# Optimization experiments

Hardware: AMD Instinct MI355X
Metric: run time of the kernel (lower is better)

Reference implementation:

```python
import jax, jax.numpy as jnp
import numpy as np

N_STREAM = 5
N_ITER = 5
P_DIMS = [240, 240, 240, 240, 240]
P = sum(P_DIMS)          # 1200
B = 128
KAPPA = 0.8
LEAKY_SLOPE = 0.01       # torch nn.LeakyReLU default


def _build_masks():
    # retrive_it_mask=True: mask[i] = ones over first sum(P_DIMS[:n_stream-i]) dims, zeros after
    rows = []
    for i in range(N_ITER):
        n_on = int(sum(P_DIMS[:N_STREAM - i]))
        rows.append(np.concatenate([np.ones(n_on, np.float32), np.zeros(P - n_on, np.float32)]))
    return jnp.asarray(np.stack(rows))  # [n_iter, P]


def f_p(x):
    # LeakyReLU(clamp(x, -1, 1))
    return jax.nn.leaky_relu(jnp.clip(x, -1.0, 1.0), negative_slope=LEAKY_SLOPE)


def setup_inputs() -> dict:
    key = jax.random.key(0)
    k1, k2 = jax.random.split(key)
    query = jax.random.normal(k1, (B, P), dtype=jnp.float32)
    # scale M so the batched GEMV doesn't saturate the clamp everywhere
    M = jax.random.normal(k2, (B, P, P), dtype=jnp.float32) * (1.0 / np.sqrt(P))
    masks = _build_masks()
    return {"query": query, "M": M, "masks": masks}


def reference(query, M, masks):
    # query: [B, P] (torch.cat of the per-stream list), M: [B, P, P], masks: [n_iter, P]
    h = f_p(query)

    def step(h, mask):
        mv = jnp.einsum('bp,bpq->bq', h, M)            # batched vector-matrix product
        h_new = (1.0 - mask) * h + mask * f_p(KAPPA * h + h * mv)
        return h_new, None

    h, _ = jax.lax.scan(step, h, masks)
    # original returns the per-stream split [h[:, n_p[f]:n_p[f+1]]]; that is a zero-cost
    # view of the concatenated h, so we return the full [B, P] tensor.
    return h
```

## Files before the change

### kernel.cpp

```cpp
#include <hip/hip_runtime.h>

namespace {

constexpr int kB = 128;
constexpr int kP = 1200;
constexpr float kKappa = 0.8f;
constexpr float kSlope = 0.01f;

__device__ __forceinline__ float f_p(float x) {
    x = fminf(1.0f, fmaxf(-1.0f, x));
    return x >= 0.0f ? x : kSlope * x;
}

__global__ __launch_bounds__(256) void init_h(const float* __restrict__ q,
                                              float* __restrict__ h) {
    int i = blockIdx.x * 256 + threadIdx.x;
    if (i < kB * kP) h[i] = f_p(q[i]);
}

__global__ __launch_bounds__(256) void iter_step(const float* __restrict__ h_in,
                                                 const float* __restrict__ M,
                                                 float* __restrict__ h_out,
                                                 int n_on) {
    const int b = blockIdx.y;
    const int tid = threadIdx.x;
    __shared__ float hs[kP];
    for (int i = tid; i < kP; i += 256) hs[i] = h_in[(size_t)b * kP + i];
    __syncthreads();

    if (blockIdx.x == 0) {
        for (int i = n_on + tid; i < kP; i += 256)
            h_out[(size_t)b * kP + i] = hs[i];
    }

    const int q = blockIdx.x * 240 + tid;
    if (tid < 240) {
        const float* Mb = M + (size_t)b * kP * kP + q;
        float acc = 0.0f;
        #pragma unroll 8
        for (int p = 0; p < kP; ++p) {
            acc = fmaf(hs[p], Mb[(size_t)p * kP], acc);
        }
        const float hq = hs[q];
        h_out[(size_t)b * kP + q] = f_p(kKappa * hq + hq * acc);
    }
}

}

extern "C" void kernel_launch(void* const* d_in, const int* in_sizes, int n_in,
                              void* d_out, int out_size, void* d_ws, size_t ws_size,
                              hipStream_t stream) {
    const float* query = (const float*)d_in[0];
    const float* M     = (const float*)d_in[1];
    float* out = (float*)d_out;
    float* w   = (float*)d_ws;

    init_h<<<dim3((kB * kP + 255) / 256), dim3(256), 0, stream>>>(query, w);

    const int n_on[5] = {1200, 960, 720, 480, 240};
    float* bufs[6] = {w, out, w, out, w, out};
    for (int it = 0; it < 5; ++it) {
        dim3 grid(n_on[it] / 240, kB);
        iter_step<<<grid, dim3(256), 0, stream>>>(bufs[it], M, bufs[it + 1], n_on[it]);
    }
}
```

Measured before the change: 1.342 ms.

## Vectorize M loads as float4 and split the reduction across waves

Each block now covers 256 output columns. Every lane loads float4 slices of M, and the four waves each reduce a 300-row slice of p, with the partial sums combined through shared memory. This is meant to widen global loads, raise memory-level parallelism with 12 loads in flight per lane, and keep more of each block's threads busy. The cost is an extra shared-memory reduction and barrier, plus clamped redundant loads for the out-of-range columns in the last tile.

```diff
diff --git a/kernel.cpp b/kernel.cpp
--- a/kernel.cpp
+++ b/kernel.cpp
@@ -23,26 +23,64 @@
                                                  float* __restrict__ h_out,
                                                  int n_on) {
     const int b = blockIdx.y;
+    const int tile = blockIdx.x;
     const int tid = threadIdx.x;
+    const int wave = tid >> 6;
+    const int lane = tid & 63;
+
     __shared__ float hs[kP];
-    for (int i = tid; i < kP; i += 256) hs[i] = h_in[(size_t)b * kP + i];
+    __shared__ float4 part[4][64];
+
+    {
+        const float4* h4 = (const float4*)(h_in + (size_t)b * kP);
+        float4* hs4 = (float4*)hs;
+        for (int i = tid; i < kP / 4; i += 256) hs4[i] = h4[i];
+    }
     __syncthreads();
 
-    if (blockIdx.x == 0) {
+    if (tile == 0) {
         for (int i = n_on + tid; i < kP; i += 256)
             h_out[(size_t)b * kP + i] = hs[i];
     }
 
-    const int q = blockIdx.x * 240 + tid;
-    if (tid < 240) {
-        const float* Mb = M + (size_t)b * kP * kP + q;
-        float acc = 0.0f;
-        #pragma unroll 8
-        for (int p = 0; p < kP; ++p) {
-            acc = fmaf(hs[p], Mb[(size_t)p * kP], acc);
+    const int cf_raw = tile * 64 + lane;
+    const int cf = min(cf_raw, kP / 4 - 1);
+    const int p0 = wave * 300;
+
+    const float4* Mp = (const float4*)(M + (size_t)b * kP * kP) +
+                       (size_t)p0 * (kP / 4) + cf;
+
+    float4 acc = make_float4(0.f, 0.f, 0.f, 0.f);
+    for (int pb = 0; pb < 300; pb += 12) {
+        float4 m[12];
+        #pragma unroll
+        for (int j = 0; j < 12; ++j) m[j] = Mp[(size_t)j * (kP / 4)];
+        float hv[12];
+        #pragma unroll
+        for (int j = 0; j < 3; ++j) {
+            float4 h4v = *(const float4*)&hs[p0 + pb + j * 4];
+            hv[j * 4 + 0] = h4v.x; hv[j * 4 + 1] = h4v.y;
+            hv[j * 4 + 2] = h4v.z; hv[j * 4 + 3] = h4v.w;
         }
+        #pragma unroll
+        for (int j = 0; j < 12; ++j) {
+            acc.x = fmaf(hv[j], m[j].x, acc.x);
+            acc.y = fmaf(hv[j], m[j].y, acc.y);
+            acc.z = fmaf(hv[j], m[j].z, acc.z);
+            acc.w = fmaf(hv[j], m[j].w, acc.w);
+        }
+        Mp += 12 * (kP / 4);
+    }
+    part[wave][lane] = acc;
+    __syncthreads();
+
+    const int q = tile * 256 + tid;
+    if (q < n_on) {
+        const float* pf = (const float*)part;
+        float mv = pf[0 * 256 + tid] + pf[1 * 256 + tid] +
+                   pf[2 * 256 + tid] + pf[3 * 256 + tid];
         const float hq = hs[q];
-        h_out[(size_t)b * kP + q] = f_p(kKappa * hq + hq * acc);
+        h_out[(size_t)b * kP + q] = f_p(kKappa * hq + hq * mv);
     }
 }
 
@@ -61,7 +99,7 @@
     const int n_on[5] = {1200, 960, 720, 480, 240};
     float* bufs[6] = {w, out, w, out, w, out};
     for (int it = 0; it < 5; ++it) {
-        dim3 grid(n_on[it] / 240, kB);
+        dim3 grid((n_on[it] + 255) / 256, kB);
         iter_step<<<grid, dim3(256), 0, stream>>>(bufs[it], M, bufs[it + 1], n_on[it]);
     }
 }
```

New measurement: 1.217 ms. 1.1x faster.
